# Kernel optimization log

Measured on AMD Instinct MI355X. Metric: run time of the kernel, lower is better.

Reference implementation:

```python
import jax, jax.numpy as jnp
import numpy as np

N, E, H, T = 50000, 100000, 512, 6  # nodes, edges, hidden_size, num_edge_types


def setup_inputs() -> dict:
    key = jax.random.key(0)
    ks = jax.random.split(key, 14)
    xav = 1.0 / np.sqrt(H)
    return {
        "statement_embeddings": jax.random.normal(ks[0], (N, H), jnp.float32),
        "source_indices": jax.random.randint(ks[1], (E,), 0, N, dtype=jnp.int32),
        "dest_indices": jax.random.randint(ks[2], (E,), 0, N, dtype=jnp.int32),
        "edge_types": jax.random.randint(ks[3], (E,), 0, T, dtype=jnp.int32),
        "num_nodes": N,
        "hidden_size": H,
        # edge_dense: Dense(features=6*H), xavier_uniform kernel, tiny-normal bias
        "W_edge": jax.random.uniform(ks[4], (H, T * H), jnp.float32, -1.0, 1.0) * np.sqrt(6.0 / (H + T * H)),
        "b_edge": jax.random.normal(ks[5], (T * H,), jnp.float32) * 1e-6,
        # GRUCell params (flax convention: input denses have bias; hidden r/z denses no bias; hidden n dense has bias)
        "W_ir": jax.random.normal(ks[6], (H, H), jnp.float32) * xav,
        "W_iz": jax.random.normal(ks[7], (H, H), jnp.float32) * xav,
        "W_in": jax.random.normal(ks[8], (H, H), jnp.float32) * xav,
        "b_ir": jnp.zeros((H,), jnp.float32),
        "b_iz": jnp.zeros((H,), jnp.float32),
        "b_in": jnp.zeros((H,), jnp.float32),
        "W_hr": jax.random.normal(ks[9], (H, H), jnp.float32) * xav,
        "W_hz": jax.random.normal(ks[10], (H, H), jnp.float32) * xav,
        "W_hn": jax.random.normal(ks[11], (H, H), jnp.float32) * xav,
        "b_hn": jnp.zeros((H,), jnp.float32),
    }


def reference(statement_embeddings, source_indices, dest_indices, edge_types,
              num_nodes, hidden_size,
              W_edge, b_edge,
              W_ir, W_iz, W_in, b_ir, b_iz, b_in,
              W_hr, W_hz, W_hn, b_hn):
    num_edge_types = 6
    # gather source node embeddings: [E, H]
    src = statement_embeddings[source_indices]
    # per-edge dense to all edge types: [E, T*H] -> [E, T, H]
    all_types = (src @ W_edge + b_edge).reshape(-1, num_edge_types, hidden_size)
    # select the slice for each edge's type: [E, H]
    msgs = jnp.take_along_axis(all_types, edge_types[:, None, None], axis=1)[:, 0, :]
    # scatter-add to destination nodes: [N, H]
    proposed = jax.ops.segment_sum(msgs, dest_indices, num_segments=num_nodes)
    # GRU update: inputs=proposed, carry=statement_embeddings
    h = statement_embeddings
    r = jax.nn.sigmoid(proposed @ W_ir + b_ir + h @ W_hr)
    z = jax.nn.sigmoid(proposed @ W_iz + b_iz + h @ W_hz)
    n = jnp.tanh(proposed @ W_in + b_in + r * (h @ W_hn + b_hn))
    return (1.0 - z) * n + z * h
```

## Files before the change

kernel.cpp:

```cpp
#include <hip/hip_runtime.h>
#include <hip/hip_bf16.h>
#include <math.h>

#define H 512
#define NT 6

#define EBM 128
#define EBN 128
#define EBK 32
#define GBM 128
#define GBN 64
#define GBK 32

#define PSCALE 65536.0f
#define PINV   (1.0f / 65536.0f)

typedef short bf16x8 __attribute__((ext_vector_type(8)));
typedef float f32x4 __attribute__((ext_vector_type(4)));

__device__ __forceinline__ float sigmoidf_(float x) { return 1.0f / (1.0f + expf(-x)); }

__device__ __forceinline__ unsigned short f2bf(float f) {
    unsigned int u = __float_as_uint(f);
    u = (u + 0x7FFF + ((u >> 16) & 1)) >> 16;
    return (unsigned short)u;
}

__device__ __forceinline__ void glds16(const void* g, void* l) {
    __builtin_amdgcn_global_load_lds((const __attribute__((address_space(1))) unsigned int*)g,
                                     (__attribute__((address_space(3))) unsigned int*)l,
                                     16, 0, 0);
}

#define WAITBAR(N)                                                        \
    {                                                                     \
        asm volatile("s_waitcnt vmcnt(" #N ") lgkmcnt(0)" ::: "memory");  \
        __builtin_amdgcn_s_barrier();                                     \
        asm volatile("" ::: "memory");                                    \
    }

__global__ void hist_kernel(const int* __restrict__ etype, int E, int* __restrict__ meta) {
    __shared__ int lh[NT];
    if (threadIdx.x < NT) lh[threadIdx.x] = 0;
    __syncthreads();
    int i = blockIdx.x * blockDim.x + threadIdx.x;
    if (i < E) atomicAdd(&lh[etype[i]], 1);
    __syncthreads();
    if (threadIdx.x < NT) {
        int c = lh[threadIdx.x];
        if (c) atomicAdd(&meta[threadIdx.x], c);
    }
}

__global__ void prefix_kernel(int* __restrict__ meta) {
    if (threadIdx.x == 0 && blockIdx.x == 0) {
        int acc = 0;
        for (int t = 0; t < NT; ++t) {
            meta[8 + t]  = acc;
            meta[16 + t] = acc;
            acc += ((meta[t] + EBM - 1) / EBM) * EBM;
        }
        meta[8 + NT] = acc;
    }
}

__global__ void scatter_perm_kernel(const int* __restrict__ etype, int E,
                                    int* __restrict__ meta, int* __restrict__ perm) {
    __shared__ int lcount[NT];
    __shared__ int lbase[NT];
    const int tid = threadIdx.x;
    if (tid < NT) lcount[tid] = 0;
    __syncthreads();
    int i = blockIdx.x * blockDim.x + tid;
    int t = 0, rank = 0;
    if (i < E) {
        t = etype[i];
        rank = atomicAdd(&lcount[t], 1);
    }
    __syncthreads();
    if (tid < NT) {
        int c = lcount[tid];
        lbase[tid] = c ? atomicAdd(&meta[16 + tid], c) : 0;
    }
    __syncthreads();
    if (i < E) perm[lbase[t] + rank] = i;
}

__global__ void conv_to_ah(const float* __restrict__ in, unsigned short* __restrict__ AH,
                           int n4, int half) {
    int i = blockIdx.x * blockDim.x + threadIdx.x;
    if (i < n4) {
        float4 v = ((const float4*)in)[i];
        ushort4 o;
        o.x = f2bf(v.x); o.y = f2bf(v.y); o.z = f2bf(v.z); o.w = f2bf(v.w);
        int row = i >> 7;
        int c4  = i & 127;
        ((ushort4*)AH)[row * 256 + half * 128 + c4] = o;
    }
}

__global__ void conv_i2ah(const int* __restrict__ in, unsigned short* __restrict__ AH, int n4) {
    int i = blockIdx.x * blockDim.x + threadIdx.x;
    if (i < n4) {
        int4 v = ((const int4*)in)[i];
        ushort4 o;
        o.x = f2bf((float)v.x * PINV); o.y = f2bf((float)v.y * PINV);
        o.z = f2bf((float)v.z * PINV); o.w = f2bf((float)v.w * PINV);
        int row = i >> 7;
        int c4  = i & 127;
        ((ushort4*)AH)[row * 256 + c4] = o;
    }
}

__global__ void conv_gru_w_kernel(const float* __restrict__ Wir, const float* __restrict__ Wiz,
                                  const float* __restrict__ Win, const float* __restrict__ Whr,
                                  const float* __restrict__ Whz, const float* __restrict__ Whn,
                                  unsigned short* __restrict__ Brt, unsigned short* __restrict__ Bzt,
                                  unsigned short* __restrict__ Bnt) {
    int idx = blockIdx.x * blockDim.x + threadIdx.x;
    if (idx >= 512 * 1024) return;
    int n = idx >> 10;
    int k = idx & 1023;
    int kk = k & 511;
    const float* wr = (k < 512) ? Wir : Whr;
    const float* wz = (k < 512) ? Wiz : Whz;
    const float* wn = (k < 512) ? Win : Whn;
    Brt[idx] = f2bf(wr[kk * H + n]);
    Bzt[idx] = f2bf(wz[kk * H + n]);
    Bnt[idx] = f2bf(wn[kk * H + n]);
}

__global__ void conv_edge_w_kernel(const float* __restrict__ W_edge, unsigned short* __restrict__ WeT) {
    int idx = blockIdx.x * blockDim.x + threadIdx.x;
    if (idx >= 3072 * 512) return;
    int n = idx >> 9;
    int k = idx & 511;
    WeT[idx] = f2bf(W_edge[(size_t)k * (NT * H) + n]);
}

__global__ __launch_bounds__(256)
void edge_msg_mfma(const unsigned short* __restrict__ AH,
                   const int* __restrict__ src_idx,
                   const int* __restrict__ dst_idx,
                   const float* __restrict__ b_edge,
                   const unsigned short* __restrict__ WeT,
                   const int* __restrict__ meta,
                   const int* __restrict__ perm,
                   int* __restrict__ proposed)
{
    __shared__ short As[3][EBM * EBK];
    __shared__ short Bs[3][EBN * EBK];
    __shared__ int ls_src[EBM];
    __shared__ int ls_dst[EBM];

    const int rowBase = blockIdx.y * EBM;
    if (rowBase >= meta[8 + NT]) return;
    int t = 0;
    while (rowBase >= meta[8 + t + 1]) ++t;

    const int colBase = blockIdx.x * EBN;
    const int tid = threadIdx.x;

    if (tid < EBM) {
        int e = perm[rowBase + tid];
        int s = 512, d = -1;
        if (e >= 0) { s = src_idx[e] * 1024 + 512; d = dst_idx[e] * H; }
        ls_src[tid] = s;
        ls_dst[tid] = d;
    }
    __syncthreads();

    const int lane = tid & 63;
    const int wave = tid >> 6;
    const int wm = (wave >> 1) * 64;
    const int wn = (wave & 1) * 64;
    const int q = lane >> 4;
    const int r = lane & 15;

    const int rA   = tid >> 2;
    const int slot = (tid & 3) * 8;

    const int s0 = ls_src[rA];
    const int s1 = ls_src[64 + rA];
    const size_t b0 = ((size_t)(t * H + colBase + rA)) * H + slot;
    const size_t b1 = ((size_t)(t * H + colBase + 64 + rA)) * H + slot;

    f32x4 acc[4][4];
    #pragma unroll
    for (int i = 0; i < 4; ++i)
        #pragma unroll
        for (int j = 0; j < 4; ++j) acc[i][j] = (f32x4){0.f, 0.f, 0.f, 0.f};

#define ESTAGE(S, B)                                                         \
    {                                                                        \
        glds16(AH + (size_t)s0 + (S) * EBK + slot, &As[B][tid * 8]);         \
        glds16(AH + (size_t)s1 + (S) * EBK + slot, &As[B][(256 + tid) * 8]); \
        glds16(WeT + b0 + (S) * EBK, &Bs[B][tid * 8]);                       \
        glds16(WeT + b1 + (S) * EBK, &Bs[B][(256 + tid) * 8]);               \
    }

#define ECOMPUTE(B)                                                                               \
    {                                                                                             \
        bf16x8 a[4];                                                                              \
        _Pragma("unroll")                                                                         \
        for (int i = 0; i < 4; ++i)                                                               \
            a[i] = *(const bf16x8*)&As[B][(wm + i * 16 + r) * EBK + q * 8];                       \
        _Pragma("unroll")                                                                         \
        for (int j = 0; j < 4; ++j) {                                                             \
            bf16x8 b = *(const bf16x8*)&Bs[B][(wn + j * 16 + r) * EBK + q * 8];                   \
            _Pragma("unroll")                                                                     \
            for (int i = 0; i < 4; ++i)                                                           \
                acc[i][j] = __builtin_amdgcn_mfma_f32_16x16x32_bf16(a[i], b, acc[i][j], 0, 0, 0); \
        }                                                                                         \
    }

#define ESTEP(S)                         \
    {                                    \
        WAITBAR(4);                      \
        ESTAGE((S) + 2, ((S) + 2) % 3);  \
        ECOMPUTE((S) % 3);               \
    }

    ESTAGE(0, 0);
    ESTAGE(1, 1);
    ESTEP(0)  ESTEP(1)  ESTEP(2)  ESTEP(3)  ESTEP(4)  ESTEP(5)  ESTEP(6)
    ESTEP(7)  ESTEP(8)  ESTEP(9)  ESTEP(10) ESTEP(11) ESTEP(12) ESTEP(13)
    { WAITBAR(4); ECOMPUTE(2); }
    { WAITBAR(0); ECOMPUTE(0); }
#undef ESTAGE
#undef ECOMPUTE
#undef ESTEP

    int cols[4];
    float bias[4];
    #pragma unroll
    for (int j = 0; j < 4; ++j) {
        cols[j] = colBase + wn + j * 16 + r;
        bias[j] = b_edge[t * H + cols[j]];
    }
    #pragma unroll
    for (int i = 0; i < 4; ++i) {
        #pragma unroll
        for (int reg = 0; reg < 4; ++reg) {
            int row = wm + i * 16 + q * 4 + reg;
            int d = ls_dst[row];
            if (d < 0) continue;
            #pragma unroll
            for (int j = 0; j < 4; ++j)
                atomicAdd(&proposed[(size_t)d + cols[j]],
                          __float2int_rn((acc[i][j][reg] + bias[j]) * PSCALE));
        }
    }
}

__global__ __launch_bounds__(256, 2)
void gru_mfma(const unsigned short* __restrict__ AH,
              const float* __restrict__ emb_f32,
              const unsigned short* __restrict__ Brt,
              const unsigned short* __restrict__ Bzt,
              const unsigned short* __restrict__ Bnt,
              const float* __restrict__ bir, const float* __restrict__ biz,
              const float* __restrict__ bin, const float* __restrict__ bhn,
              float* __restrict__ out, int N)
{
    __shared__ short As[3][GBM * GBK];
    __shared__ short Brs[3][GBN * GBK];
    __shared__ short Bzs[3][GBN * GBK];
    __shared__ short Bns[3][GBN * GBK];

    int wg = blockIdx.y * gridDim.x + blockIdx.x;
    const int nwg = gridDim.x * gridDim.y;
    if ((nwg & 7) == 0) {
        const int cpx = nwg >> 3;
        wg = (wg & 7) * cpx + (wg >> 3);
    }
    const int rowBase = (wg / gridDim.x) * GBM;
    const int colBase = (wg % gridDim.x) * GBN;

    const int tid = threadIdx.x;
    const int lane = tid & 63;
    const int wave = tid >> 6;
    const int wm = (wave >> 1) * 64;
    const int wn = (wave & 1) * 32;
    const int q = lane >> 4;
    const int r = lane & 15;

    const int rA   = tid >> 2;
    const int slot = (tid & 3) * 8;

    const size_t aOff0 = (size_t)(rowBase + rA) * 1024 + slot;
    const size_t aOff1 = (size_t)(rowBase + 64 + rA) * 1024 + slot;
    const size_t bOff  = (size_t)(colBase + rA) * 1024 + slot;

    f32x4 accR[4][2], accZ[4][2], accNI[4][2], accNH[4][2];
    #pragma unroll
    for (int i = 0; i < 4; ++i)
        #pragma unroll
        for (int j = 0; j < 2; ++j) {
            accR[i][j] = (f32x4){0.f, 0.f, 0.f, 0.f};
            accZ[i][j] = accR[i][j];
            accNI[i][j] = accR[i][j];
            accNH[i][j] = accR[i][j];
        }

#define GSTAGE(S, B)                                             \
    {                                                            \
        glds16(AH + aOff0 + (S) * GBK, &As[B][tid * 8]);         \
        glds16(AH + aOff1 + (S) * GBK, &As[B][(256 + tid) * 8]); \
        glds16(Brt + bOff + (S) * GBK, &Brs[B][tid * 8]);        \
        glds16(Bzt + bOff + (S) * GBK, &Bzs[B][tid * 8]);        \
        glds16(Bnt + bOff + (S) * GBK, &Bns[B][tid * 8]);        \
    }

#define GCOMPUTE(ACCN, B)                                                                            \
    {                                                                                                \
        bf16x8 a[4];                                                                                 \
        _Pragma("unroll")                                                                            \
        for (int i = 0; i < 4; ++i)                                                                  \
            a[i] = *(const bf16x8*)&As[B][(wm + i * 16 + r) * GBK + q * 8];                          \
        _Pragma("unroll")                                                                            \
        for (int j = 0; j < 2; ++j) {                                                                \
            bf16x8 br = *(const bf16x8*)&Brs[B][(wn + j * 16 + r) * GBK + q * 8];                    \
            bf16x8 bz = *(const bf16x8*)&Bzs[B][(wn + j * 16 + r) * GBK + q * 8];                    \
            bf16x8 bn = *(const bf16x8*)&Bns[B][(wn + j * 16 + r) * GBK + q * 8];                    \
            _Pragma("unroll")                                                                        \
            for (int i = 0; i < 4; ++i) {                                                            \
                accR[i][j] = __builtin_amdgcn_mfma_f32_16x16x32_bf16(a[i], br, accR[i][j], 0, 0, 0); \
                accZ[i][j] = __builtin_amdgcn_mfma_f32_16x16x32_bf16(a[i], bz, accZ[i][j], 0, 0, 0); \
                ACCN[i][j] = __builtin_amdgcn_mfma_f32_16x16x32_bf16(a[i], bn, ACCN[i][j], 0, 0, 0); \
            }                                                                                        \
        }                                                                                            \
    }

#define GSTEP(S, ACCN)                   \
    {                                    \
        WAITBAR(5);                      \
        GSTAGE((S) + 2, ((S) + 2) % 3);  \
        GCOMPUTE(ACCN, (S) % 3);         \
    }

    GSTAGE(0, 0);
    GSTAGE(1, 1);
    GSTEP(0,  accNI) GSTEP(1,  accNI) GSTEP(2,  accNI) GSTEP(3,  accNI)
    GSTEP(4,  accNI) GSTEP(5,  accNI) GSTEP(6,  accNI) GSTEP(7,  accNI)
    GSTEP(8,  accNI) GSTEP(9,  accNI) GSTEP(10, accNI) GSTEP(11, accNI)
    GSTEP(12, accNI) GSTEP(13, accNI) GSTEP(14, accNI) GSTEP(15, accNI)
    GSTEP(16, accNH) GSTEP(17, accNH) GSTEP(18, accNH) GSTEP(19, accNH)
    GSTEP(20, accNH) GSTEP(21, accNH) GSTEP(22, accNH) GSTEP(23, accNH)
    GSTEP(24, accNH) GSTEP(25, accNH) GSTEP(26, accNH) GSTEP(27, accNH)
    GSTEP(28, accNH) GSTEP(29, accNH)
    { WAITBAR(5); GCOMPUTE(accNH, 0); }
    { WAITBAR(0); GCOMPUTE(accNH, 1); }
#undef GSTAGE
#undef GCOMPUTE
#undef GSTEP

    #pragma unroll
    for (int j = 0; j < 2; ++j) {
        const int col = colBase + wn + j * 16 + r;
        const float vbir = bir[col], vbiz = biz[col], vbin = bin[col], vbhn = bhn[col];
        #pragma unroll
        for (int i = 0; i < 4; ++i) {
            #pragma unroll
            for (int reg = 0; reg < 4; ++reg) {
                const int row = rowBase + wm + i * 16 + q * 4 + reg;
                if (row >= N) continue;
                float rg = sigmoidf_(accR[i][j][reg] + vbir);
                float zg = sigmoidf_(accZ[i][j][reg] + vbiz);
                float ng = tanhf(accNI[i][j][reg] + vbin + rg * (accNH[i][j][reg] + vbhn));
                float h = emb_f32[(size_t)row * H + col];
                out[(size_t)row * H + col] = (1.0f - zg) * ng + zg * h;
            }
        }
    }
}

extern "C" void kernel_launch(void* const* d_in, const int* in_sizes, int n_in,
                              void* d_out, int out_size, void* d_ws, size_t ws_size,
                              hipStream_t stream) {
    const float* emb     = (const float*)d_in[0];
    const int*   src_idx = (const int*)d_in[1];
    const int*   dst_idx = (const int*)d_in[2];
    const int*   etype   = (const int*)d_in[3];
    const float* W_edge  = (const float*)d_in[6];
    const float* b_edge  = (const float*)d_in[7];
    const float* Wir = (const float*)d_in[8];
    const float* Wiz = (const float*)d_in[9];
    const float* Win = (const float*)d_in[10];
    const float* bir = (const float*)d_in[11];
    const float* biz = (const float*)d_in[12];
    const float* bin = (const float*)d_in[13];
    const float* Whr = (const float*)d_in[14];
    const float* Whz = (const float*)d_in[15];
    const float* Whn = (const float*)d_in[16];
    const float* bhn = (const float*)d_in[17];

    const int E = in_sizes[1];
    const int N = in_sizes[0] / H;
    const int NH = N * H;

    char* ws = (char*)d_ws;
    int*            proposed = (int*)ws;                         ws += (size_t)NH * 4;
    unsigned short* AH       = (unsigned short*)ws;              ws += (size_t)NH * 2 * 2;
    unsigned short* Brt      = (unsigned short*)ws;              ws += 512 * 1024 * 2;
    unsigned short* Bzt      = (unsigned short*)ws;              ws += 512 * 1024 * 2;
    unsigned short* Bnt      = (unsigned short*)ws;              ws += 512 * 1024 * 2;
    unsigned short* WeT      = (unsigned short*)ws;              ws += 3072 * 512 * 2;
    int*            meta     = (int*)ws;                         ws += 32 * 4;
    int*            perm     = (int*)ws;
    const int maxRowTiles = (E + EBM - 1) / EBM + NT;

    hipMemsetAsync(proposed, 0, (size_t)NH * 4, stream);
    hipMemsetAsync(meta, 0, 32 * 4, stream);
    hipMemsetAsync(perm, 0xFF, (size_t)maxRowTiles * EBM * 4, stream);

    const int n4 = NH / 4;
    conv_to_ah<<<(n4 + 255) / 256, 256, 0, stream>>>(emb, AH, n4, 1);
    conv_gru_w_kernel<<<(512 * 1024 + 255) / 256, 256, 0, stream>>>(
        Wir, Wiz, Win, Whr, Whz, Whn, Brt, Bzt, Bnt);
    conv_edge_w_kernel<<<(3072 * 512 + 255) / 256, 256, 0, stream>>>(W_edge, WeT);

    hist_kernel<<<(E + 255) / 256, 256, 0, stream>>>(etype, E, meta);
    prefix_kernel<<<1, 64, 0, stream>>>(meta);
    scatter_perm_kernel<<<(E + 255) / 256, 256, 0, stream>>>(etype, E, meta, perm);

    dim3 egrid(H / EBN, maxRowTiles);
    edge_msg_mfma<<<egrid, 256, 0, stream>>>(AH, src_idx, dst_idx, b_edge, WeT,
                                             meta, perm, proposed);

    conv_i2ah<<<(n4 + 255) / 256, 256, 0, stream>>>(proposed, AH, n4);

    dim3 ggrid(H / GBN, (N + GBM - 1) / GBM);
    gru_mfma<<<ggrid, 256, 0, stream>>>(AH, emb, Brt, Bzt, Bnt,
                                        bir, biz, bin, bhn, (float*)d_out, N);
}
```

Measured before the change: 781.6 us.

## Widen edge GEMM tile, swizzle LDS layout, and remap blocks column-major per XCD

Widens the edge-message GEMM tile from 128 to 256 columns, so each gathered source-row tile is reused across twice as many output columns and fewer blocks redo the gather. Adds an XOR swizzle to the LDS staging layout in both the edge and GRU kernels to reduce bank conflicts on the MFMA operand reads. Replaces the block mapping with a column-major, per-XCD contiguous assignment in both kernels to improve L2 locality of the weight tiles. In exchange the edge kernel now holds twice as many accumulators per thread under a two-blocks-per-CU launch bound, which raises register pressure and risks spills. The grid dimension on the host side must also match the new tile width.

```diff
diff --git a/kernel.cpp b/kernel.cpp
--- a/kernel.cpp
+++ b/kernel.cpp
@@ -6,7 +6,7 @@
 #define NT 6
 
 #define EBM 128
-#define EBN 128
+#define EBN 256
 #define EBK 32
 #define GBM 128
 #define GBN 64
@@ -38,6 +38,17 @@
         __builtin_amdgcn_s_barrier();                                     \
         asm volatile("" ::: "memory");                                    \
     }
+
+__device__ __forceinline__ void xcd_colmajor_map(int gx, int gy, int* rowT, int* colT) {
+    const int nwg = gx * gy;
+    const int bid = (int)(blockIdx.y * gridDim.x + blockIdx.x);
+    const int x = bid & 7;
+    const int o = bid >> 3;
+    const int q = nwg >> 3, rr = nwg & 7;
+    const int L = (x < rr) ? x * (q + 1) + o : rr * (q + 1) + (x - rr) * q + o;
+    *colT = L / gy;
+    *rowT = L % gy;
+}
 
 __global__ void hist_kernel(const int* __restrict__ etype, int E, int* __restrict__ meta) {
     __shared__ int lh[NT];
@@ -138,7 +149,7 @@
     WeT[idx] = f2bf(W_edge[(size_t)k * (NT * H) + n]);
 }
 
-__global__ __launch_bounds__(256)
+__global__ __launch_bounds__(256, 2)
 void edge_msg_mfma(const unsigned short* __restrict__ AH,
                    const int* __restrict__ src_idx,
                    const int* __restrict__ dst_idx,
@@ -153,12 +164,14 @@
     __shared__ int ls_src[EBM];
     __shared__ int ls_dst[EBM];
 
-    const int rowBase = blockIdx.y * EBM;
+    int rowT, colT;
+    xcd_colmajor_map(gridDim.x, gridDim.y, &rowT, &colT);
+    const int rowBase = rowT * EBM;
     if (rowBase >= meta[8 + NT]) return;
     int t = 0;
     while (rowBase >= meta[8 + t + 1]) ++t;
 
-    const int colBase = blockIdx.x * EBN;
+    const int colBase = colT * EBN;
     const int tid = threadIdx.x;
 
     if (tid < EBM) {
@@ -173,30 +186,32 @@
     const int lane = tid & 63;
     const int wave = tid >> 6;
     const int wm = (wave >> 1) * 64;
-    const int wn = (wave & 1) * 64;
+    const int wn = (wave & 1) * 128;
     const int q = lane >> 4;
     const int r = lane & 15;
 
-    const int rA   = tid >> 2;
-    const int slot = (tid & 3) * 8;
-
-    const int s0 = ls_src[rA];
-    const int s1 = ls_src[64 + rA];
-    const size_t b0 = ((size_t)(t * H + colBase + rA)) * H + slot;
-    const size_t b1 = ((size_t)(t * H + colBase + 64 + rA)) * H + slot;
-
-    f32x4 acc[4][4];
+    const int rA = tid >> 2;
+    const int gs = (((tid & 3) ^ ((rA >> 1) & 3)) * 8);
+    const int qs8 = ((q ^ ((r >> 1) & 3)) * 8);
+
+    const size_t s0 = (size_t)ls_src[rA] + gs;
+    const size_t s1 = (size_t)ls_src[64 + rA] + gs;
+    const size_t bB = ((size_t)(t * H + colBase + rA)) * H + gs;
+
+    f32x4 acc[4][8];
     #pragma unroll
     for (int i = 0; i < 4; ++i)
         #pragma unroll
-        for (int j = 0; j < 4; ++j) acc[i][j] = (f32x4){0.f, 0.f, 0.f, 0.f};
-
-#define ESTAGE(S, B)                                                         \
-    {                                                                        \
-        glds16(AH + (size_t)s0 + (S) * EBK + slot, &As[B][tid * 8]);         \
-        glds16(AH + (size_t)s1 + (S) * EBK + slot, &As[B][(256 + tid) * 8]); \
-        glds16(WeT + b0 + (S) * EBK, &Bs[B][tid * 8]);                       \
-        glds16(WeT + b1 + (S) * EBK, &Bs[B][(256 + tid) * 8]);               \
+        for (int j = 0; j < 8; ++j) acc[i][j] = (f32x4){0.f, 0.f, 0.f, 0.f};
+
+#define ESTAGE(S, B)                                                          \
+    {                                                                         \
+        glds16(AH + s0 + (S) * EBK, &As[B][tid * 8]);                         \
+        glds16(AH + s1 + (S) * EBK, &As[B][(256 + tid) * 8]);                 \
+        glds16(WeT + bB + (S) * EBK,                 &Bs[B][tid * 8]);        \
+        glds16(WeT + bB + 64 * H + (S) * EBK,  &Bs[B][(256 + tid) * 8]);      \
+        glds16(WeT + bB + 128 * H + (S) * EBK, &Bs[B][(512 + tid) * 8]);      \
+        glds16(WeT + bB + 192 * H + (S) * EBK, &Bs[B][(768 + tid) * 8]);      \
     }
 
 #define ECOMPUTE(B)                                                                               \
@@ -204,37 +219,32 @@
         bf16x8 a[4];                                                                              \
         _Pragma("unroll")                                                                         \
         for (int i = 0; i < 4; ++i)                                                               \
-            a[i] = *(const bf16x8*)&As[B][(wm + i * 16 + r) * EBK + q * 8];                       \
+            a[i] = *(const bf16x8*)&As[B][(wm + i * 16 + r) * EBK + qs8];                         \
         _Pragma("unroll")                                                                         \
-        for (int j = 0; j < 4; ++j) {                                                             \
-            bf16x8 b = *(const bf16x8*)&Bs[B][(wn + j * 16 + r) * EBK + q * 8];                   \
+        for (int j = 0; j < 8; ++j) {                                                             \
+            bf16x8 b = *(const bf16x8*)&Bs[B][(wn + j * 16 + r) * EBK + qs8];                     \
             _Pragma("unroll")                                                                     \
             for (int i = 0; i < 4; ++i)                                                           \
                 acc[i][j] = __builtin_amdgcn_mfma_f32_16x16x32_bf16(a[i], b, acc[i][j], 0, 0, 0); \
         }                                                                                         \
     }
 
-#define ESTEP(S)                         \
-    {                                    \
-        WAITBAR(4);                      \
-        ESTAGE((S) + 2, ((S) + 2) % 3);  \
-        ECOMPUTE((S) % 3);               \
-    }
-
     ESTAGE(0, 0);
     ESTAGE(1, 1);
-    ESTEP(0)  ESTEP(1)  ESTEP(2)  ESTEP(3)  ESTEP(4)  ESTEP(5)  ESTEP(6)
-    ESTEP(7)  ESTEP(8)  ESTEP(9)  ESTEP(10) ESTEP(11) ESTEP(12) ESTEP(13)
-    { WAITBAR(4); ECOMPUTE(2); }
+    for (int s = 0; s < 14; ++s) {
+        WAITBAR(6);
+        ESTAGE(s + 2, (s + 2) % 3);
+        ECOMPUTE(s % 3);
+    }
+    { WAITBAR(6); ECOMPUTE(2); }
     { WAITBAR(0); ECOMPUTE(0); }
 #undef ESTAGE
 #undef ECOMPUTE
-#undef ESTEP
-
-    int cols[4];
-    float bias[4];
+
+    int cols[8];
+    float bias[8];
     #pragma unroll
-    for (int j = 0; j < 4; ++j) {
+    for (int j = 0; j < 8; ++j) {
         cols[j] = colBase + wn + j * 16 + r;
         bias[j] = b_edge[t * H + cols[j]];
     }
@@ -246,7 +256,7 @@
             int d = ls_dst[row];
             if (d < 0) continue;
             #pragma unroll
-            for (int j = 0; j < 4; ++j)
+            for (int j = 0; j < 8; ++j)
                 atomicAdd(&proposed[(size_t)d + cols[j]],
                           __float2int_rn((acc[i][j][reg] + bias[j]) * PSCALE));
         }
@@ -268,14 +278,10 @@
     __shared__ short Bzs[3][GBN * GBK];
     __shared__ short Bns[3][GBN * GBK];
 
-    int wg = blockIdx.y * gridDim.x + blockIdx.x;
-    const int nwg = gridDim.x * gridDim.y;
-    if ((nwg & 7) == 0) {
-        const int cpx = nwg >> 3;
-        wg = (wg & 7) * cpx + (wg >> 3);
-    }
-    const int rowBase = (wg / gridDim.x) * GBM;
-    const int colBase = (wg % gridDim.x) * GBN;
+    int rowT, colT;
+    xcd_colmajor_map(gridDim.x, gridDim.y, &rowT, &colT);
+    const int rowBase = rowT * GBM;
+    const int colBase = colT * GBN;
 
     const int tid = threadIdx.x;
     const int lane = tid & 63;
@@ -285,12 +291,13 @@
     const int q = lane >> 4;
     const int r = lane & 15;
 
-    const int rA   = tid >> 2;
-    const int slot = (tid & 3) * 8;
-
-    const size_t aOff0 = (size_t)(rowBase + rA) * 1024 + slot;
-    const size_t aOff1 = (size_t)(rowBase + 64 + rA) * 1024 + slot;
-    const size_t bOff  = (size_t)(colBase + rA) * 1024 + slot;
+    const int rA = tid >> 2;
+    const int gs = (((tid & 3) ^ ((rA >> 1) & 3)) * 8);
+    const int qs8 = ((q ^ ((r >> 1) & 3)) * 8);
+
+    const size_t aOff0 = (size_t)(rowBase + rA) * 1024 + gs;
+    const size_t aOff1 = (size_t)(rowBase + 64 + rA) * 1024 + gs;
+    const size_t bOff  = (size_t)(colBase + rA) * 1024 + gs;
 
     f32x4 accR[4][2], accZ[4][2], accNI[4][2], accNH[4][2];
     #pragma unroll
@@ -317,12 +324,12 @@
         bf16x8 a[4];                                                                                 \
         _Pragma("unroll")                                                                            \
         for (int i = 0; i < 4; ++i)                                                                  \
-            a[i] = *(const bf16x8*)&As[B][(wm + i * 16 + r) * GBK + q * 8];                          \
+            a[i] = *(const bf16x8*)&As[B][(wm + i * 16 + r) * GBK + qs8];                            \
         _Pragma("unroll")                                                                            \
         for (int j = 0; j < 2; ++j) {                                                                \
-            bf16x8 br = *(const bf16x8*)&Brs[B][(wn + j * 16 + r) * GBK + q * 8];                    \
-            bf16x8 bz = *(const bf16x8*)&Bzs[B][(wn + j * 16 + r) * GBK + q * 8];                    \
-            bf16x8 bn = *(const bf16x8*)&Bns[B][(wn + j * 16 + r) * GBK + q * 8];                    \
+            bf16x8 br = *(const bf16x8*)&Brs[B][(wn + j * 16 + r) * GBK + qs8];                      \
+            bf16x8 bz = *(const bf16x8*)&Bzs[B][(wn + j * 16 + r) * GBK + qs8];                      \
+            bf16x8 bn = *(const bf16x8*)&Bns[B][(wn + j * 16 + r) * GBK + qs8];                      \
             _Pragma("unroll")                                                                        \
             for (int i = 0; i < 4; ++i) {                                                            \
                 accR[i][j] = __builtin_amdgcn_mfma_f32_16x16x32_bf16(a[i], br, accR[i][j], 0, 0, 0); \
```

Result: slower. 803.1 us (+2.7%).
